# Kernel optimization log

Measured on AMD Instinct MI355X. Metric: run time of the kernel, lower is better.

## Reference

```python
import jax, jax.numpy as jnp
import numpy as np
from jax.ops import segment_sum, segment_max

N, E, G = 20000, 100000, 16
TILE, EMB, HID, OUT, FEAT, HEADS = 32, 128, 256, 512, 512, 8
SLOPE = 0.2


def setup_inputs() -> dict:
    key = jax.random.key(0)
    ks = jax.random.split(key, 20)
    def gn(k, shape, fan_in):
        return jax.random.normal(k, shape, jnp.float32) * (1.0 / np.sqrt(fan_in))
    return {
        "x": jax.random.normal(ks[0], (N, TILE), jnp.float32),
        "edge_index": jax.random.randint(ks[1], (2, E), 0, N, jnp.int32),
        "batch": jnp.sort(jax.random.randint(ks[2], (N,), 0, G, jnp.int32)),
        "W0": gn(ks[3], (TILE, EMB), TILE), "b0": jnp.zeros((EMB,), jnp.float32),
        "W1": gn(ks[4], (EMB, HEADS * HID), EMB),
        "a1s": gn(ks[5], (HEADS, HID), HID), "a1d": gn(ks[6], (HEADS, HID), HID),
        "b1": jnp.zeros((HEADS * HID,), jnp.float32),
        "W2": gn(ks[7], (HEADS * HID, HEADS * HID), HEADS * HID),
        "a2s": gn(ks[8], (HEADS, HID), HID), "a2d": gn(ks[9], (HEADS, HID), HID),
        "b2": jnp.zeros((HEADS * HID,), jnp.float32),
        "W3": gn(ks[10], (HEADS * HID, OUT), HEADS * HID),
        "a3s": gn(ks[11], (1, OUT), OUT), "a3d": gn(ks[12], (1, OUT), OUT),
        "b3": jnp.zeros((OUT,), jnp.float32),
        "Wf": gn(ks[13], (OUT, FEAT), OUT), "bf": jnp.zeros((FEAT,), jnp.float32),
    }


def gat_conv(x, src, dst, W, a_s, a_d, b, heads, ch, n):
    # PyG GATConv: linear, per-edge additive attention, segment softmax over dst, scatter-add
    h = (x @ W).reshape(n, heads, ch)                       # [N,H,C]
    e_src = jnp.einsum("nhc,hc->nh", h, a_s)                 # [N,H]
    e_dst = jnp.einsum("nhc,hc->nh", h, a_d)
    e = jax.nn.leaky_relu(e_src[src] + e_dst[dst], SLOPE)    # [E,H]
    m = segment_max(e, dst, num_segments=n)                  # [N,H]
    m = jax.lax.stop_gradient(jnp.where(jnp.isfinite(m), m, 0.0))
    ex = jnp.exp(e - m[dst])
    den = segment_sum(ex, dst, num_segments=n)
    alpha = ex / (den[dst] + 1e-16)                          # [E,H]
    out = segment_sum(h[src] * alpha[..., None], dst, num_segments=n)  # [N,H,C]
    return out.reshape(n, heads * ch) + b


def reference(x, edge_index, batch, W0, b0, W1, a1s, a1d, b1, W2, a2s, a2d, b2,
              W3, a3s, a3d, b3, Wf, bf):
    loop = jnp.arange(N, dtype=edge_index.dtype)             # PyG adds self-loops by default
    src = jnp.concatenate([edge_index[0], loop])
    dst = jnp.concatenate([edge_index[1], loop])
    h = jax.nn.leaky_relu(x @ W0 + b0, SLOPE)
    h = jax.nn.leaky_relu(gat_conv(h, src, dst, W1, a1s, a1d, b1, HEADS, HID, N), SLOPE)
    h = jax.nn.leaky_relu(gat_conv(h, src, dst, W2, a2s, a2d, b2, HEADS, HID, N), SLOPE)
    h = jax.nn.leaky_relu(gat_conv(h, src, dst, W3, a3s, a3d, b3, 1, OUT, N), SLOPE)
    sums = segment_sum(h, batch, num_segments=G)             # global_mean_pool
    cnt = segment_sum(jnp.ones((N,), h.dtype), batch, num_segments=G)
    mean = sums / jnp.maximum(cnt, 1.0)[:, None]
    return jax.nn.leaky_relu(mean @ Wf + bf, SLOPE)
```

## Files before the change

kernel.cpp:

```cpp
#include <hip/hip_runtime.h>
#include <hip/hip_bf16.h>

#define N_NODES 20000
#define N_EDGES 100000
#define ET (N_EDGES + N_NODES)
#define G_GRAPHS 16
#define SLOPE 0.2f

using short8  = __attribute__((ext_vector_type(8))) short;
using floatx4 = __attribute__((ext_vector_type(4))) float;

__device__ __forceinline__ float lrelu(float x) { return x > 0.f ? x : SLOPE * x; }

__device__ __forceinline__ float b2f(unsigned short u) {
    union { unsigned int i; float f; } v; v.i = ((unsigned int)u) << 16; return v.f;
}
__device__ __forceinline__ unsigned short f2b(float f) {
    union { float f; unsigned int i; } v; v.f = f;
    unsigned int i = v.i;
    return (unsigned short)((i + 0x7fffu + ((i >> 16) & 1u)) >> 16);
}

__device__ __forceinline__ void gld16(const void* g, void* l) {
    __builtin_amdgcn_global_load_lds((const __attribute__((address_space(1))) void*)g,
                                     (__attribute__((address_space(3))) void*)l, 16, 0, 0);
}

__device__ int dev_lower_bound(const int* a, int n, int key) {
    int lo = 0, hi = n;
    while (lo < hi) { int mid = (lo + hi) >> 1; if (a[mid] < key) lo = mid + 1; else hi = mid; }
    return lo;
}

__global__ void zero_kernel(int* __restrict__ p, int n) {
    int i = blockIdx.x * blockDim.x + threadIdx.x;
    if (i < n) p[i] = 0;
}

__global__ void count_kernel(const int* __restrict__ ei, int* __restrict__ counts) {
    int e = blockIdx.x * blockDim.x + threadIdx.x;
    if (e >= ET) return;
    int dst = (e < N_EDGES) ? ei[N_EDGES + e] : (e - N_EDGES);
    atomicAdd(&counts[dst], 1);
}

__global__ void scan_kernel(const int* __restrict__ counts, int* __restrict__ row_ptr) {
    __shared__ int sums[256];
    int t = threadIdx.x;
    const int CH = (N_NODES + 255) / 256;
    int base = t * CH;
    int s = 0;
    for (int i = 0; i < CH; i++) { int idx = base + i; if (idx < N_NODES) s += counts[idx]; }
    sums[t] = s;
    __syncthreads();
    for (int off = 1; off < 256; off <<= 1) {
        int v = (t >= off) ? sums[t - off] : 0;
        __syncthreads();
        sums[t] += v;
        __syncthreads();
    }
    int run = (t == 0) ? 0 : sums[t - 1];
    for (int i = 0; i < CH; i++) {
        int idx = base + i;
        if (idx < N_NODES) { row_ptr[idx] = run; run += counts[idx]; }
    }
    if (t == 255) row_ptr[N_NODES] = run;
}

__global__ void fill_kernel(const int* __restrict__ ei, const int* __restrict__ row_ptr,
                            int* __restrict__ fill_cnt, int* __restrict__ col) {
    int e = blockIdx.x * blockDim.x + threadIdx.x;
    if (e >= ET) return;
    int src, dst;
    if (e < N_EDGES) { src = ei[e]; dst = ei[N_EDGES + e]; }
    else             { src = dst = e - N_EDGES; }
    int pos = atomicAdd(&fill_cnt[dst], 1);
    col[row_ptr[dst] + pos] = src;
}

__global__ void transpose_kernel(const float* __restrict__ W, unsigned short* __restrict__ Wt,
                                 int K, int N) {
    __shared__ float tile[32][33];
    int bn = blockIdx.x * 32, bk = blockIdx.y * 32;
    int tx = threadIdx.x & 31, ty = threadIdx.x >> 5;
#pragma unroll
    for (int p = 0; p < 32; p += 8)
        tile[ty + p][tx] = W[(size_t)(bk + ty + p) * N + bn + tx];
    __syncthreads();
#pragma unroll
    for (int p = 0; p < 32; p += 8)
        Wt[(size_t)(bn + ty + p) * K + bk + tx] = f2b(tile[tx][ty + p]);
}

__global__ void gemm0_kernel(const float* __restrict__ x, const float* __restrict__ W0,
                             const float* __restrict__ b0, unsigned short* __restrict__ h0) {
    __shared__ float xr[32];
    int n = blockIdx.x, t = threadIdx.x;
    if (t < 32) xr[t] = x[n * 32 + t];
    __syncthreads();
    float acc = 0.f;
#pragma unroll
    for (int k = 0; k < 32; k++) acc += xr[k] * W0[k * 128 + t];
    h0[(size_t)n * 128 + t] = f2b(lrelu(acc + b0[t]));
}

__global__ __launch_bounds__(256) void gemm_mfma(const unsigned short* __restrict__ A,
                                                 const unsigned short* __restrict__ Bt,
                                                 unsigned short* __restrict__ C,
                                                 int M, int N, int K,
                                                 const float* __restrict__ a_s,
                                                 const float* __restrict__ a_d,
                                                 float* __restrict__ es,
                                                 float* __restrict__ ed,
                                                 int H, int head_ch) {
    __shared__ __align__(16) unsigned short As[128][32];
    __shared__ __align__(16) unsigned short Bs[128][32];
    int t = threadIdx.x;
    int w = t >> 6, l = t & 63;
    int r0 = blockIdx.y * 128, c0 = blockIdx.x * 128;
    int wr = (w >> 1) * 64, wc = (w & 1) * 64;
    int lrow = l >> 2;
    int gcb  = (l & 3) ^ ((l >> 3) & 3);
    int m16 = l & 15, qb = l >> 4;
    int sw  = (m16 >> 1) & 3;
    int roff = ((qb ^ sw) * 8);
    floatx4 acc[4][4] = {};

    for (int k0 = 0; k0 < K; k0 += 32) {
        __syncthreads();
#pragma unroll
        for (int q = 0; q < 2; q++) {
            int row = w * 32 + q * 16 + lrow;
            int ga = min(r0 + row, M - 1);
            gld16(A + (size_t)ga * K + k0 + gcb * 8, &As[w * 32 + q * 16][0]);
            gld16(Bt + (size_t)(c0 + row) * K + k0 + gcb * 8, &Bs[w * 32 + q * 16][0]);
        }
        __syncthreads();
        short8 af[4], bfr[4];
#pragma unroll
        for (int i = 0; i < 4; i++) af[i] = *(const short8*)&As[wr + i * 16 + m16][roff];
#pragma unroll
        for (int j = 0; j < 4; j++) bfr[j] = *(const short8*)&Bs[wc + j * 16 + m16][roff];
#pragma unroll
        for (int i = 0; i < 4; i++)
#pragma unroll
            for (int j = 0; j < 4; j++)
                acc[i][j] = __builtin_amdgcn_mfma_f32_16x16x32_bf16(bfr[j], af[i], acc[i][j], 0, 0, 0);
    }
    int quad = l >> 4;
#pragma unroll
    for (int i = 0; i < 4; i++) {
        int r = r0 + wr + i * 16 + m16;
        if (r < M) {
#pragma unroll
            for (int j = 0; j < 4; j++) {
                int c = c0 + wc + j * 16 + quad * 4;
                ushort4 o = make_ushort4(f2b(acc[i][j][0]), f2b(acc[i][j][1]),
                                         f2b(acc[i][j][2]), f2b(acc[i][j][3]));
                *(ushort4*)&C[(size_t)r * N + c] = o;
            }
        }
    }
    int base = c0 + wc;
    int hd = base / head_ch;
    int boff = base - hd * head_ch;
    const float* asr = a_s + hd * head_ch + boff;
    const float* adr = a_d + hd * head_ch + boff;
#pragma unroll
    for (int i = 0; i < 4; i++) {
        int r = r0 + wr + i * 16 + m16;
        float s1 = 0.f, s2 = 0.f;
#pragma unroll
        for (int j = 0; j < 4; j++)
#pragma unroll
            for (int reg = 0; reg < 4; reg++) {
                int cc = j * 16 + quad * 4 + reg;
                float av = acc[i][j][reg];
                s1 += av * asr[cc];
                s2 += av * adr[cc];
            }
        s1 += __shfl_xor(s1, 16); s2 += __shfl_xor(s2, 16);
        s1 += __shfl_xor(s1, 32); s2 += __shfl_xor(s2, 32);
        if (quad == 0 && r < M) {
            atomicAdd(&es[r * H + hd], s1);
            atomicAdd(&ed[r * H + hd], s2);
        }
    }
}

template <int H, int C>
__global__ __launch_bounds__(256) void agg_wave(const unsigned short* __restrict__ hmid,
                                                const float* __restrict__ es,
                                                const float* __restrict__ ed,
                                                const int* __restrict__ row_ptr,
                                                const int* __restrict__ col,
                                                const float* __restrict__ bias,
                                                unsigned short* __restrict__ out) {
    constexpr int HC = H * C;
    constexpr int CH = HC / 512;
    int wv = threadIdx.x >> 6, l = threadIdx.x & 63;
    int v = blockIdx.x * 4 + wv;
    if (v >= N_NODES) return;
    int rs = row_ptr[v], deg = row_ptr[v + 1] - rs;
    int hd[CH];
    float edv[CH], den[CH], acc[CH][8];
#pragma unroll
    for (int c = 0; c < CH; c++) {
        hd[c] = (c * 512 + l * 8) / C;
        edv[c] = ed[v * H + hd[c]];
        den[c] = 0.f;
#pragma unroll
        for (int k = 0; k < 8; k++) acc[c][k] = 0.f;
    }
    int sN = (deg > 0) ? col[rs] : 0;
    for (int e = 0; e < deg; e++) {
        int s = sN;
        if (e + 1 < deg) sN = col[rs + e + 1];
        const unsigned short* hr = hmid + (size_t)s * HC + l * 8;
        uint4 u[CH];
#pragma unroll
        for (int c = 0; c < CH; c++) u[c] = *(const uint4*)(hr + c * 512);
        float ex[CH];
#pragma unroll
        for (int c = 0; c < CH; c++) {
            ex[c] = __expf(lrelu(es[s * H + hd[c]] + edv[c]));
            den[c] += ex[c];
        }
#pragma unroll
        for (int c = 0; c < CH; c++) {
            float a = ex[c];
            acc[c][0] += a * b2f((unsigned short)(u[c].x & 0xffff));
            acc[c][1] += a * b2f((unsigned short)(u[c].x >> 16));
            acc[c][2] += a * b2f((unsigned short)(u[c].y & 0xffff));
            acc[c][3] += a * b2f((unsigned short)(u[c].y >> 16));
            acc[c][4] += a * b2f((unsigned short)(u[c].z & 0xffff));
            acc[c][5] += a * b2f((unsigned short)(u[c].z >> 16));
            acc[c][6] += a * b2f((unsigned short)(u[c].w & 0xffff));
            acc[c][7] += a * b2f((unsigned short)(u[c].w >> 16));
        }
    }
#pragma unroll
    for (int c = 0; c < CH; c++) {
        float inv = 1.f / (den[c] + 1e-16f);
        unsigned short o[8];
#pragma unroll
        for (int k = 0; k < 8; k++)
            o[k] = f2b(lrelu(acc[c][k] * inv + bias[c * 512 + l * 8 + k]));
        *(uint4*)&out[(size_t)v * HC + c * 512 + l * 8] = *(const uint4*)o;
    }
}

__global__ void pool_kernel(const unsigned short* __restrict__ h3, const int* __restrict__ batch,
                            float* __restrict__ msum) {
    int b0 = blockIdx.x * 128, t = threadIdx.x;
    int nend = min(b0 + 128, N_NODES);
    int curg = batch[b0];
    float s0 = 0.f, s1 = 0.f;
    for (int n = b0; n < nend; n++) {
        int g = batch[n];
        if (g != curg) {
            atomicAdd(&msum[curg * 512 + t * 2], s0);
            atomicAdd(&msum[curg * 512 + t * 2 + 1], s1);
            s0 = s1 = 0.f; curg = g;
        }
        unsigned int u = *(const unsigned int*)&h3[(size_t)n * 512 + t * 2];
        s0 += b2f((unsigned short)(u & 0xffff));
        s1 += b2f((unsigned short)(u >> 16));
    }
    atomicAdd(&msum[curg * 512 + t * 2], s0);
    atomicAdd(&msum[curg * 512 + t * 2 + 1], s1);
}

__global__ void final_kernel(const float* __restrict__ msum, const int* __restrict__ batch,
                             const float* __restrict__ Wf, const float* __restrict__ bf,
                             float* __restrict__ out) {
    int g = blockIdx.x, t = threadIdx.x;
    __shared__ float mr[512];
    __shared__ float sinv;
    if (t == 0) {
        int st = dev_lower_bound(batch, N_NODES, g);
        int en = dev_lower_bound(batch, N_NODES, g + 1);
        sinv = 1.f / fmaxf((float)(en - st), 1.f);
    }
    __syncthreads();
    for (int c = t; c < 512; c += 256) mr[c] = msum[g * 512 + c] * sinv;
    __syncthreads();
    for (int j = t; j < 512; j += 256) {
        float s = 0.f;
        for (int k = 0; k < 512; k++) s += mr[k] * Wf[k * 512 + j];
        out[g * 512 + j] = lrelu(s + bf[j]);
    }
}

extern "C" void kernel_launch(void* const* d_in, const int* in_sizes, int n_in,
                              void* d_out, int out_size, void* d_ws, size_t ws_size,
                              hipStream_t stream) {
    const float* x   = (const float*)d_in[0];
    const int*   ei  = (const int*)d_in[1];
    const int*   bat = (const int*)d_in[2];
    const float* W0  = (const float*)d_in[3];
    const float* b0  = (const float*)d_in[4];
    const float* W1  = (const float*)d_in[5];
    const float* a1s = (const float*)d_in[6];
    const float* a1d = (const float*)d_in[7];
    const float* b1  = (const float*)d_in[8];
    const float* W2  = (const float*)d_in[9];
    const float* a2s = (const float*)d_in[10];
    const float* a2d = (const float*)d_in[11];
    const float* b2  = (const float*)d_in[12];
    const float* W3  = (const float*)d_in[13];
    const float* a3s = (const float*)d_in[14];
    const float* a3d = (const float*)d_in[15];
    const float* b3  = (const float*)d_in[16];
    const float* Wf  = (const float*)d_in[17];
    const float* bf  = (const float*)d_in[18];
    float* out = (float*)d_out;

    char* p = (char*)d_ws;
    unsigned short* bufA = (unsigned short*)p; p += (size_t)N_NODES * 2048 * 2;
    unsigned short* bufB = (unsigned short*)p; p += (size_t)N_NODES * 2048 * 2;
    unsigned short* h0   = (unsigned short*)p; p += (size_t)N_NODES * 128 * 2;
    unsigned short* W1t  = (unsigned short*)p; p += (size_t)2048 * 128 * 2;
    unsigned short* W2t  = (unsigned short*)p; p += (size_t)2048 * 2048 * 2;
    unsigned short* W3t  = (unsigned short*)p; p += (size_t)512 * 2048 * 2;
    float* zreg = (float*)p;
    float* es1 = (float*)p; p += (size_t)N_NODES * 8 * 4;
    float* ed1 = (float*)p; p += (size_t)N_NODES * 8 * 4;
    float* es2 = (float*)p; p += (size_t)N_NODES * 8 * 4;
    float* ed2 = (float*)p; p += (size_t)N_NODES * 8 * 4;
    float* es3 = (float*)p; p += (size_t)N_NODES * 4;
    float* ed3 = (float*)p; p += (size_t)N_NODES * 4;
    float* msum = (float*)p; p += 16 * 512 * 4;
    const int ZN = N_NODES * 8 * 4 + N_NODES * 2 + 16 * 512;
    int* counts  = (int*)p; p += (size_t)N_NODES * 4;
    int* row_ptr = (int*)p; p += (size_t)(N_NODES + 1) * 4;
    int* col     = (int*)p; p += (size_t)ET * 4;

    zero_kernel<<<(N_NODES + 255) / 256, 256, 0, stream>>>(counts, N_NODES);
    count_kernel<<<(ET + 255) / 256, 256, 0, stream>>>(ei, counts);
    scan_kernel<<<1, 256, 0, stream>>>(counts, row_ptr);
    zero_kernel<<<(N_NODES + 255) / 256, 256, 0, stream>>>(counts, N_NODES);
    fill_kernel<<<(ET + 255) / 256, 256, 0, stream>>>(ei, row_ptr, counts, col);

    transpose_kernel<<<dim3(2048 / 32, 128 / 32), 256, 0, stream>>>(W1, W1t, 128, 2048);
    transpose_kernel<<<dim3(2048 / 32, 2048 / 32), 256, 0, stream>>>(W2, W2t, 2048, 2048);
    transpose_kernel<<<dim3(512 / 32, 2048 / 32), 256, 0, stream>>>(W3, W3t, 2048, 512);

    zero_kernel<<<(ZN + 255) / 256, 256, 0, stream>>>((int*)zreg, ZN);

    gemm0_kernel<<<N_NODES, 128, 0, stream>>>(x, W0, b0, h0);

    dim3 g12(2048 / 128, (N_NODES + 127) / 128);
    dim3 g3(512 / 128, (N_NODES + 127) / 128);
    int aggb = (N_NODES + 3) / 4;

    gemm_mfma<<<g12, 256, 0, stream>>>(h0, W1t, bufB, N_NODES, 2048, 128,
                                       a1s, a1d, es1, ed1, 8, 256);
    agg_wave<8, 256><<<aggb, 256, 0, stream>>>(bufB, es1, ed1, row_ptr, col, b1, bufA);

    gemm_mfma<<<g12, 256, 0, stream>>>(bufA, W2t, bufB, N_NODES, 2048, 2048,
                                       a2s, a2d, es2, ed2, 8, 256);
    agg_wave<8, 256><<<aggb, 256, 0, stream>>>(bufB, es2, ed2, row_ptr, col, b2, bufA);

    gemm_mfma<<<g3, 256, 0, stream>>>(bufA, W3t, bufB, N_NODES, 512, 2048,
                                      a3s, a3d, es3, ed3, 1, 512);
    agg_wave<1, 512><<<aggb, 256, 0, stream>>>(bufB, es3, ed3, row_ptr, col, b3, bufA);

    pool_kernel<<<(N_NODES + 127) / 128, 256, 0, stream>>>(bufA, bat, msum);
    final_kernel<<<G_GRAPHS, 256, 0, stream>>>(msum, bat, Wf, bf, out);
}
```

Baseline: 881.4 us.

## Aggregate layer-1 inputs before the per-head GEMM and split out attention-score kernels

Layer 1 now uses linearity: the 128-wide input features are softmax-aggregated per head first, and the per-head GEMM with K=128 runs afterwards, with bias and leaky-relu fused into its epilogue. Attention logits for layer 1 come from W1 folded with a1s/a1d, so nothing needs the 2048-wide hidden tensor. This replaces the wide 2048-column edge gather with a 128-column one. Layers 2 and 3 drop the atomic attention epilogue from the GEMM and compute scores in separate per-node kernels. That removes the atomics and zeroing but adds an extra read of the hidden tensor.

```diff
diff --git a/kernel.cpp b/kernel.cpp
--- a/kernel.cpp
+++ b/kernel.cpp
@@ -104,15 +104,76 @@
     h0[(size_t)n * 128 + t] = f2b(lrelu(acc + b0[t]));
 }
 
+__global__ void wes_kernel(const float* __restrict__ W1, const float* __restrict__ a1s,
+                           const float* __restrict__ a1d, float* __restrict__ w_es,
+                           float* __restrict__ w_ed) {
+    int hd = blockIdx.x;
+    int k  = threadIdx.x;
+    const float* w  = W1 + (size_t)k * 2048 + hd * 256;
+    const float* as_ = a1s + hd * 256;
+    const float* ad_ = a1d + hd * 256;
+    float s1 = 0.f, s2 = 0.f;
+    for (int c = 0; c < 256; c++) { float wv = w[c]; s1 += wv * as_[c]; s2 += wv * ad_[c]; }
+    w_es[k * 8 + hd] = s1;
+    w_ed[k * 8 + hd] = s2;
+}
+
+__global__ void es1_kernel(const unsigned short* __restrict__ h0, const float* __restrict__ w_es,
+                           const float* __restrict__ w_ed, float* __restrict__ es,
+                           float* __restrict__ ed) {
+    int n = blockIdx.x, t = threadIdx.x;
+    int hd = t >> 5, l = t & 31;
+    uint2 u = *(const uint2*)&h0[(size_t)n * 128 + l * 4];
+    float x0 = b2f((unsigned short)(u.x & 0xffff)), x1 = b2f((unsigned short)(u.x >> 16));
+    float x2 = b2f((unsigned short)(u.y & 0xffff)), x3 = b2f((unsigned short)(u.y >> 16));
+    int k0 = l * 4;
+    float s1 = x0 * w_es[(k0 + 0) * 8 + hd] + x1 * w_es[(k0 + 1) * 8 + hd] +
+               x2 * w_es[(k0 + 2) * 8 + hd] + x3 * w_es[(k0 + 3) * 8 + hd];
+    float s2 = x0 * w_ed[(k0 + 0) * 8 + hd] + x1 * w_ed[(k0 + 1) * 8 + hd] +
+               x2 * w_ed[(k0 + 2) * 8 + hd] + x3 * w_ed[(k0 + 3) * 8 + hd];
+    for (int m = 16; m >= 1; m >>= 1) { s1 += __shfl_xor(s1, m); s2 += __shfl_xor(s2, m); }
+    if (l == 0) { es[n * 8 + hd] = s1; ed[n * 8 + hd] = s2; }
+}
+
+__global__ __launch_bounds__(256) void agg1_wave(const unsigned short* __restrict__ h0,
+                                                 const float* __restrict__ es,
+                                                 const float* __restrict__ ed,
+                                                 const int* __restrict__ row_ptr,
+                                                 const int* __restrict__ col,
+                                                 unsigned short* __restrict__ outp) {
+    int wv = threadIdx.x >> 6, l = threadIdx.x & 63;
+    int v = blockIdx.x * 4 + wv;
+    if (v >= N_NODES) return;
+    int rs = row_ptr[v], deg = row_ptr[v + 1] - rs;
+    float edv[8], den[8], a0[8], a1[8];
+#pragma unroll
+    for (int hd = 0; hd < 8; hd++) { edv[hd] = ed[v * 8 + hd]; den[hd] = 0.f; a0[hd] = 0.f; a1[hd] = 0.f; }
+    int sN = (deg > 0) ? col[rs] : 0;
+    for (int e = 0; e < deg; e++) {
+        int s = sN;
+        if (e + 1 < deg) sN = col[rs + e + 1];
+        unsigned int u = *(const unsigned int*)&h0[(size_t)s * 128 + l * 2];
+        float x0 = b2f((unsigned short)(u & 0xffff)), x1 = b2f((unsigned short)(u >> 16));
+#pragma unroll
+        for (int hd = 0; hd < 8; hd++) {
+            float a = __expf(lrelu(es[s * 8 + hd] + edv[hd]));
+            den[hd] += a;
+            a0[hd] += a * x0;
+            a1[hd] += a * x1;
+        }
+    }
+#pragma unroll
+    for (int hd = 0; hd < 8; hd++) {
+        float inv = 1.f / (den[hd] + 1e-16f);
+        unsigned int o = (unsigned int)f2b(a0[hd] * inv) | ((unsigned int)f2b(a1[hd] * inv) << 16);
+        *(unsigned int*)&outp[(size_t)v * 1024 + hd * 128 + l * 2] = o;
+    }
+}
+
 __global__ __launch_bounds__(256) void gemm_mfma(const unsigned short* __restrict__ A,
                                                  const unsigned short* __restrict__ Bt,
                                                  unsigned short* __restrict__ C,
-                                                 int M, int N, int K,
-                                                 const float* __restrict__ a_s,
-                                                 const float* __restrict__ a_d,
-                                                 float* __restrict__ es,
-                                                 float* __restrict__ ed,
-                                                 int H, int head_ch) {
+                                                 int M, int N, int K) {
     __shared__ __align__(16) unsigned short As[128][32];
     __shared__ __align__(16) unsigned short Bs[128][32];
     int t = threadIdx.x;
@@ -161,31 +222,104 @@
             }
         }
     }
-    int base = c0 + wc;
-    int hd = base / head_ch;
-    int boff = base - hd * head_ch;
-    const float* asr = a_s + hd * head_ch + boff;
-    const float* adr = a_d + hd * head_ch + boff;
+}
+
+__global__ __launch_bounds__(256) void gemm_mfma_h1(const unsigned short* __restrict__ A,
+                                                    const unsigned short* __restrict__ Bt,
+                                                    const float* __restrict__ bias,
+                                                    unsigned short* __restrict__ C,
+                                                    int M) {
+    const int N = 2048, K = 128;
+    __shared__ __align__(16) unsigned short As[128][32];
+    __shared__ __align__(16) unsigned short Bs[128][32];
+    int t = threadIdx.x;
+    int w = t >> 6, l = t & 63;
+    int r0 = blockIdx.y * 128, c0 = blockIdx.x * 128;
+    int wr = (w >> 1) * 64, wc = (w & 1) * 64;
+    int lrow = l >> 2;
+    int gcb  = (l & 3) ^ ((l >> 3) & 3);
+    int m16 = l & 15, qb = l >> 4;
+    int sw  = (m16 >> 1) & 3;
+    int roff = ((qb ^ sw) * 8);
+    int aoff = (c0 >> 8) * 128;
+    floatx4 acc[4][4] = {};
+
+    for (int k0 = 0; k0 < K; k0 += 32) {
+        __syncthreads();
+#pragma unroll
+        for (int q = 0; q < 2; q++) {
+            int row = w * 32 + q * 16 + lrow;
+            int ga = min(r0 + row, M - 1);
+            gld16(A + (size_t)ga * 1024 + aoff + k0 + gcb * 8, &As[w * 32 + q * 16][0]);
+            gld16(Bt + (size_t)(c0 + row) * K + k0 + gcb * 8, &Bs[w * 32 + q * 16][0]);
+        }
+        __syncthreads();
+        short8 af[4], bfr[4];
+#pragma unroll
+        for (int i = 0; i < 4; i++) af[i] = *(const short8*)&As[wr + i * 16 + m16][roff];
+#pragma unroll
+        for (int j = 0; j < 4; j++) bfr[j] = *(const short8*)&Bs[wc + j * 16 + m16][roff];
+#pragma unroll
+        for (int i = 0; i < 4; i++)
+#pragma unroll
+            for (int j = 0; j < 4; j++)
+                acc[i][j] = __builtin_amdgcn_mfma_f32_16x16x32_bf16(bfr[j], af[i], acc[i][j], 0, 0, 0);
+    }
+    int quad = l >> 4;
 #pragma unroll
     for (int i = 0; i < 4; i++) {
         int r = r0 + wr + i * 16 + m16;
-        float s1 = 0.f, s2 = 0.f;
-#pragma unroll
-        for (int j = 0; j < 4; j++)
-#pragma unroll
-            for (int reg = 0; reg < 4; reg++) {
-                int cc = j * 16 + quad * 4 + reg;
-                float av = acc[i][j][reg];
-                s1 += av * asr[cc];
-                s2 += av * adr[cc];
+        if (r < M) {
+#pragma unroll
+            for (int j = 0; j < 4; j++) {
+                int c = c0 + wc + j * 16 + quad * 4;
+                ushort4 o = make_ushort4(f2b(lrelu(acc[i][j][0] + bias[c + 0])),
+                                         f2b(lrelu(acc[i][j][1] + bias[c + 1])),
+                                         f2b(lrelu(acc[i][j][2] + bias[c + 2])),
+                                         f2b(lrelu(acc[i][j][3] + bias[c + 3])));
+                *(ushort4*)&C[(size_t)r * N + c] = o;
             }
-        s1 += __shfl_xor(s1, 16); s2 += __shfl_xor(s2, 16);
-        s1 += __shfl_xor(s1, 32); s2 += __shfl_xor(s2, 32);
-        if (quad == 0 && r < M) {
-            atomicAdd(&es[r * H + hd], s1);
-            atomicAdd(&ed[r * H + hd], s2);
-        }
-    }
+        }
+    }
+}
+
+__global__ void att8_kernel(const unsigned short* __restrict__ h, const float* __restrict__ a_s,
+                            const float* __restrict__ a_d, float* __restrict__ es,
+                            float* __restrict__ ed) {
+    int n = blockIdx.x, t = threadIdx.x;
+    int hd = t >> 5, l = t & 31;
+    const unsigned short* hr = h + (size_t)n * 2048 + hd * 256 + l * 8;
+    const float* as_ = a_s + hd * 256 + l * 8;
+    const float* ad_ = a_d + hd * 256 + l * 8;
+    uint4 u = *(const uint4*)hr;
+    float v[8] = { b2f((unsigned short)(u.x & 0xffff)), b2f((unsigned short)(u.x >> 16)),
+                   b2f((unsigned short)(u.y & 0xffff)), b2f((unsigned short)(u.y >> 16)),
+                   b2f((unsigned short)(u.z & 0xffff)), b2f((unsigned short)(u.z >> 16)),
+                   b2f((unsigned short)(u.w & 0xffff)), b2f((unsigned short)(u.w >> 16)) };
+    float s1 = 0.f, s2 = 0.f;
+#pragma unroll
+    for (int j = 0; j < 8; j++) { s1 += v[j] * as_[j]; s2 += v[j] * ad_[j]; }
+    for (int m = 16; m >= 1; m >>= 1) { s1 += __shfl_xor(s1, m); s2 += __shfl_xor(s2, m); }
+    if (l == 0) { es[n * 8 + hd] = s1; ed[n * 8 + hd] = s2; }
+}
+
+__global__ void att1_kernel(const unsigned short* __restrict__ h, const float* __restrict__ a_s,
+                            const float* __restrict__ a_d, float* __restrict__ es,
+                            float* __restrict__ ed) {
+    int n = blockIdx.x, l = threadIdx.x;
+    const unsigned short* hr = h + (size_t)n * 512 + l * 8;
+    const float* as_ = a_s + l * 8;
+    const float* ad_ = a_d + l * 8;
+    uint4 u = *(const uint4*)hr;
+    float v[8] = { b2f((unsigned short)(u.x & 0xffff)), b2f((unsigned short)(u.x >> 16)),
+                   b2f((unsigned short)(u.y & 0xffff)), b2f((unsigned short)(u.y >> 16)),
+                   b2f((unsigned short)(u.z & 0xffff)), b2f((unsigned short)(u.z >> 16)),
+                   b2f((unsigned short)(u.w & 0xffff)), b2f((unsigned short)(u.w >> 16)) };
+    float s1 = 0.f, s2 = 0.f;
+#pragma unroll
+    for (int j = 0; j < 8; j++) { s1 += v[j] * as_[j]; s2 += v[j] * ad_[j]; }
+    for (int m = 32; m >= 1; m >>= 1) { s1 += __shfl_xor(s1, m); s2 += __shfl_xor(s2, m); }
+    if (l == 0) { es[n] = s1; ed[n] = s2; }
 }
 
 template <int H, int C>
@@ -323,15 +457,11 @@
     unsigned short* W1t  = (unsigned short*)p; p += (size_t)2048 * 128 * 2;
     unsigned short* W2t  = (unsigned short*)p; p += (size_t)2048 * 2048 * 2;
     unsigned short* W3t  = (unsigned short*)p; p += (size_t)512 * 2048 * 2;
-    float* zreg = (float*)p;
-    float* es1 = (float*)p; p += (size_t)N_NODES * 8 * 4;
-    float* ed1 = (float*)p; p += (size_t)N_NODES * 8 * 4;
-    float* es2 = (float*)p; p += (size_t)N_NODES * 8 * 4;
-    float* ed2 = (float*)p; p += (size_t)N_NODES * 8 * 4;
-    float* es3 = (float*)p; p += (size_t)N_NODES * 4;
-    float* ed3 = (float*)p; p += (size_t)N_NODES * 4;
+    float* es   = (float*)p; p += (size_t)N_NODES * 8 * 4;
+    float* ed   = (float*)p; p += (size_t)N_NODES * 8 * 4;
+    float* w_es = (float*)p; p += 128 * 8 * 4;
+    float* w_ed = (float*)p; p += 128 * 8 * 4;
     float* msum = (float*)p; p += 16 * 512 * 4;
-    const int ZN = N_NODES * 8 * 4 + N_NODES * 2 + 16 * 512;
     int* counts  = (int*)p; p += (size_t)N_NODES * 4;
     int* row_ptr = (int*)p; p += (size_t)(N_NODES + 1) * 4;
     int* col     = (int*)p; p += (size_t)ET * 4;
@@ -346,7 +476,9 @@
     transpose_kernel<<<dim3(2048 / 32, 2048 / 32), 256, 0, stream>>>(W2, W2t, 2048, 2048);
     transpose_kernel<<<dim3(512 / 32, 2048 / 32), 256, 0, stream>>>(W3, W3t, 2048, 512);
 
-    zero_kernel<<<(ZN + 255) / 256, 256, 0, stream>>>((int*)zreg, ZN);
+    wes_kernel<<<8, 128, 0, stream>>>(W1, a1s, a1d, w_es, w_ed);
+
+    zero_kernel<<<(16 * 512 + 255) / 256, 256, 0, stream>>>((int*)msum, 16 * 512);
 
     gemm0_kernel<<<N_NODES, 128, 0, stream>>>(x, W0, b0, h0);
 
@@ -354,17 +486,17 @@
     dim3 g3(512 / 128, (N_NODES + 127) / 128);
     int aggb = (N_NODES + 3) / 4;
 
-    gemm_mfma<<<g12, 256, 0, stream>>>(h0, W1t, bufB, N_NODES, 2048, 128,
-                                       a1s, a1d, es1, ed1, 8, 256);
-    agg_wave<8, 256><<<aggb, 256, 0, stream>>>(bufB, es1, ed1, row_ptr, col, b1, bufA);
-
-    gemm_mfma<<<g12, 256, 0, stream>>>(bufA, W2t, bufB, N_NODES, 2048, 2048,
-                                       a2s, a2d, es2, ed2, 8, 256);
-    agg_wave<8, 256><<<aggb, 256, 0, stream>>>(bufB, es2, ed2, row_ptr, col, b2, bufA);
-
-    gemm_mfma<<<g3, 256, 0, stream>>>(bufA, W3t, bufB, N_NODES, 512, 2048,
-                                      a3s, a3d, es3, ed3, 1, 512);
-    agg_wave<1, 512><<<aggb, 256, 0, stream>>>(bufB, es3, ed3, row_ptr, col, b3, bufA);
+    es1_kernel<<<N_NODES, 256, 0, stream>>>(h0, w_es, w_ed, es, ed);
+    agg1_wave<<<aggb, 256, 0, stream>>>(h0, es, ed, row_ptr, col, bufB);
+    gemm_mfma_h1<<<g12, 256, 0, stream>>>(bufB, W1t, b1, bufA, N_NODES);
+
+    gemm_mfma<<<g12, 256, 0, stream>>>(bufA, W2t, bufB, N_NODES, 2048, 2048);
+    att8_kernel<<<N_NODES, 256, 0, stream>>>(bufB, a2s, a2d, es, ed);
+    agg_wave<8, 256><<<aggb, 256, 0, stream>>>(bufB, es, ed, row_ptr, col, b2, bufA);
+
+    gemm_mfma<<<g3, 256, 0, stream>>>(bufA, W3t, bufB, N_NODES, 512, 2048);
+    att1_kernel<<<N_NODES, 64, 0, stream>>>(bufB, a3s, a3d, es, ed);
+    agg_wave<1, 512><<<aggb, 256, 0, stream>>>(bufB, es, ed, row_ptr, col, b3, bufA);
 
     pool_kernel<<<(N_NODES + 127) / 128, 256, 0, stream>>>(bufA, bat, msum);
     final_kernel<<<G_GRAPHS, 256, 0, stream>>>(msum, bat, Wf, bf, out);
```

Result: faster. 828.5 us (-6.0%).
